# Optimization experiments

Hardware: AMD Instinct MI355X
Metric: run time of the kernel (lower is better)

## Reference

```python
import jax, jax.numpy as jnp
import numpy as np

RATIO = 4
NUM_UPSAMPLES = 2  # log2(RATIO)
PADDING = 11       # (23 - 1) // 2


def _make_kernel():
    cdf23 = 2.0 * np.array([0.5, 0.305334091185, 0.0, -0.072698593239, 0.0,
                            0.021809577942, 0.0, -0.005192756653, 0.0,
                            0.000807762146, 0.0, -6.0081482e-05])
    d = cdf23[::-1]
    base = np.insert(cdf23, 0, d[:-1])  # length 23, symmetric
    return jnp.asarray(base, dtype=jnp.float32)


def setup_inputs() -> dict:
    key = jax.random.key(0)
    x = jax.random.normal(key, (4, 8, 256, 256), dtype=jnp.float32)
    return {"x": x, "kernel": _make_kernel()}


def _sep_circ_conv(img, kernel):
    """Depthwise separable 23-tap conv with circular padding.
    img: (bs, c, h, w). Processes all (b,c) slices as one batched conv."""
    bs, c, h, w = img.shape
    flat = img.reshape(bs * c, 1, h, w)
    # horizontal pass
    ph = jnp.pad(flat, ((0, 0), (0, 0), (0, 0), (PADDING, PADDING)), mode="wrap")
    kh = kernel.reshape(1, 1, 1, -1)
    fh = jax.lax.conv_general_dilated(ph, kh, (1, 1), "VALID",
                                      dimension_numbers=("NCHW", "OIHW", "NCHW"))
    # vertical pass
    pv = jnp.pad(fh, ((0, 0), (0, 0), (PADDING, PADDING), (0, 0)), mode="wrap")
    kv = kernel.reshape(1, 1, -1, 1)
    fv = jax.lax.conv_general_dilated(pv, kv, (1, 1), "VALID",
                                      dimension_numbers=("NCHW", "OIHW", "NCHW"))
    return fv.reshape(bs, c, h, w)


def reference(x, kernel):
    cur = x
    for k in range(NUM_UPSAMPLES):
        bs, c, h, w = cur.shape
        up = jnp.zeros((bs, c, 2 * h, 2 * w), dtype=cur.dtype)
        off = 1 if k == 0 else 0  # first stage inserts at odd positions
        up = up.at[..., off::2, off::2].set(cur)
        cur = _sep_circ_conv(up, kernel)
    return cur
```

## Files before the change

### kernel.cpp

```cpp
#include <hip/hip_runtime.h>


#define SINS 50
#define SMS 132

__global__ void compute_g(const float* __restrict__ kern, float* __restrict__ gbuf) {
    const int u = threadIdx.x;
    const int s = u - 34;
    int jlo = (s - 11 + 1) >> 1;
    int jhi = (s + 11) >> 1;
    if (jlo < -11) jlo = -11;
    if (jhi > 11) jhi = 11;
    float acc = 0.f;
    for (int j = jlo; j <= jhi; ++j)
        acc += kern[11 + s - 2 * j] * kern[11 + j];
    gbuf[u] = acc;
}

__device__ inline void fma4(float4& a, float t, const float4& r) {
    a.x += t * r.x; a.y += t * r.y; a.z += t * r.z; a.w += t * r.w;
}

__global__ __launch_bounds__(256, 4) void up4_fused(
    const float* __restrict__ in, const float* __restrict__ gbuf,
    float* __restrict__ out) {
    __shared__ float sG[80];
    __shared__ __attribute__((aligned(16))) float sMid[49][SMS];
    __shared__ float sIn[49][SINS];

    const int tid = threadIdx.x;
    const int tX = blockIdx.x, tY = blockIdx.y, ch = blockIdx.z;
    const int W4 = 1024;

    if (tid < 80) sG[tid] = gbuf[tid];

    const float* inC = in + (size_t)ch * 256 * 256;
    const int N0y = 32 * tY - 9, N0x = 32 * tX - 9;
#pragma unroll
    for (int it = 0; it < 9; ++it) {
        const int idx = tid + it * 256;
        const int pi = 1 + idx / 48, pj = 1 + idx % 48;
        const int gi = (N0y + pi + 256) & 255;
        const int gj = (N0x + pj + 256) & 255;
        sIn[pi][pj] = inC[gi * 256 + gj];
    }
    __syncthreads();

    float tapA[17], tC6[6];
#pragma unroll
    for (int k = 0; k < 17; ++k) tapA[k] = sG[1 + 4 * k];
#pragma unroll
    for (int m = 0; m < 6; ++m) tC6[m] = sG[12 + 4 * m];

#pragma unroll
    for (int it = 0; it < 6; ++it) {
        const int idx = tid + it * 256;
        const int c = idx & 31, row = 1 + (idx >> 5);
        float a0 = 0.f, a1 = 0.f, a2 = 0.f, a3 = 0.f;
#pragma unroll
        for (int k = 0; k < 17; ++k) {
            const float w = sIn[row][c + 17 - k];
            a1 += tapA[k] * w;
            a3 += tapA[16 - k] * w;
            if (k >= 3 && k <= 14) {
                const int m = k - 3;
                a0 += tC6[m < 6 ? m : 11 - m] * w;
            }
            if (k == 8) a2 = w;
        }
        float4 v; v.x = a0; v.y = a1; v.z = a2; v.w = a3;
        *(float4*)&sMid[row][4 * c] = v;
    }
    __syncthreads();

    const int c = tid & 31, gp = tid >> 5;
    float4 A[4][4];
#pragma unroll
    for (int i = 0; i < 4; ++i)
#pragma unroll
        for (int p = 0; p < 4; ++p) { A[i][p].x = 0.f; A[i][p].y = 0.f; A[i][p].z = 0.f; A[i][p].w = 0.f; }

#pragma unroll
    for (int d = 1; d <= 20; ++d) {
        const float4 R = *(const float4*)&sMid[4 * gp + d][4 * c];
#pragma unroll
        for (int i = 0; i < 4; ++i) {
            const int k = i + 17 - d;
            if (k < 0 || k > 16) continue;
            fma4(A[i][1], tapA[k], R);
            fma4(A[i][3], tapA[16 - k], R);
            if (k >= 3 && k <= 14) {
                const int m = k - 3;
                fma4(A[i][0], tC6[m < 6 ? m : 11 - m], R);
            }
            if (k == 8) A[i][2] = R;
        }
    }

    float* outC = out + (size_t)ch * 1024 * 1024;
    const int row0 = 128 * tY + 16 * gp, col = 128 * tX + 4 * c;
#pragma unroll
    for (int i = 0; i < 4; ++i)
#pragma unroll
        for (int p = 0; p < 4; ++p)
            *(float4*)&outC[(size_t)(row0 + 4 * i + p) * W4 + col] = A[i][p];
}

extern "C" void kernel_launch(void* const* d_in, const int* in_sizes, int n_in,
                              void* d_out, int out_size, void* d_ws, size_t ws_size,
                              hipStream_t stream) {
    const float* x    = (const float*)d_in[0];
    const float* kern = (const float*)d_in[1];
    float* out  = (float*)d_out;
    float* gbuf = (float*)d_ws;

    compute_g<<<dim3(1), dim3(80), 0, stream>>>(kern, gbuf);
    dim3 grid(8, 8, 32);
    up4_fused<<<grid, dim3(256), 0, stream>>>(x, gbuf, out);
}
```

Before: 146.3 us.

## Fold tap precompute into main kernel, vectorize input tile loads and horizontal pass

Drops the separate compute_g launch and has each block compute the combined 80-tap filter into shared memory. Input tiles are loaded with float4 global reads when the tile does not wrap horizontally, with a scalar fallback for wrapped tiles. The horizontal pass now has each thread load a 20-float register window and produce 4 output columns, which cuts shared-memory reads. The shared arrays lose the unused halo row. The trade-off is that every block redundantly recomputes the taps and the window uses more registers.

Result: slower. 149.3 us (+2.0%).

```diff
diff --git a/kernel.cpp b/kernel.cpp
--- a/kernel.cpp
+++ b/kernel.cpp
@@ -1,48 +1,59 @@
 #include <hip/hip_runtime.h>
 
 
-#define SINS 50
+#define SINS 52
 #define SMS 132
-
-__global__ void compute_g(const float* __restrict__ kern, float* __restrict__ gbuf) {
-    const int u = threadIdx.x;
-    const int s = u - 34;
-    int jlo = (s - 11 + 1) >> 1;
-    int jhi = (s + 11) >> 1;
-    if (jlo < -11) jlo = -11;
-    if (jhi > 11) jhi = 11;
-    float acc = 0.f;
-    for (int j = jlo; j <= jhi; ++j)
-        acc += kern[11 + s - 2 * j] * kern[11 + j];
-    gbuf[u] = acc;
-}
 
 __device__ inline void fma4(float4& a, float t, const float4& r) {
     a.x += t * r.x; a.y += t * r.y; a.z += t * r.z; a.w += t * r.w;
 }
 
 __global__ __launch_bounds__(256, 4) void up4_fused(
-    const float* __restrict__ in, const float* __restrict__ gbuf,
+    const float* __restrict__ in, const float* __restrict__ kern,
     float* __restrict__ out) {
     __shared__ float sG[80];
-    __shared__ __attribute__((aligned(16))) float sMid[49][SMS];
-    __shared__ float sIn[49][SINS];
+    __shared__ __attribute__((aligned(16))) float sMid[48][SMS];
+    __shared__ __attribute__((aligned(16))) float sIn[48][SINS];
 
     const int tid = threadIdx.x;
     const int tX = blockIdx.x, tY = blockIdx.y, ch = blockIdx.z;
     const int W4 = 1024;
 
-    if (tid < 80) sG[tid] = gbuf[tid];
+    if (tid < 80) {
+        const int s = tid - 34;
+        int jlo = (s - 10) >> 1;
+        int jhi = (s + 11) >> 1;
+        if (jlo < -11) jlo = -11;
+        if (jhi > 11) jhi = 11;
+        float acc = 0.f;
+        for (int j = jlo; j <= jhi; ++j)
+            acc += kern[11 + s - 2 * j] * kern[11 + j];
+        sG[tid] = acc;
+    }
 
     const float* inC = in + (size_t)ch * 256 * 256;
     const int N0y = 32 * tY - 9, N0x = 32 * tX - 9;
+    const int gj0 = (N0x + 1) & 255;
+    if (gj0 <= 208) {
 #pragma unroll
-    for (int it = 0; it < 9; ++it) {
-        const int idx = tid + it * 256;
-        const int pi = 1 + idx / 48, pj = 1 + idx % 48;
-        const int gi = (N0y + pi + 256) & 255;
-        const int gj = (N0x + pj + 256) & 255;
-        sIn[pi][pj] = inC[gi * 256 + gj];
+        for (int it = 0; it < 3; ++it) {
+            const int idx = tid + it * 256;
+            if (idx < 576) {
+                const int pi = idx / 12, m = idx % 12;
+                const int gi = (N0y + 1 + pi + 256) & 255;
+                *(float4*)&sIn[pi][4 * m] =
+                    *(const float4*)&inC[gi * 256 + gj0 + 4 * m];
+            }
+        }
+    } else {
+#pragma unroll
+        for (int it = 0; it < 9; ++it) {
+            const int idx = tid + it * 256;
+            const int pi = idx / 48, pj = idx % 48;
+            const int gi = (N0y + 1 + pi + 256) & 255;
+            const int gj = (N0x + 1 + pj + 256) & 255;
+            sIn[pi][pj] = inC[gi * 256 + gj];
+        }
     }
     __syncthreads();
 
@@ -53,23 +64,32 @@
     for (int m = 0; m < 6; ++m) tC6[m] = sG[12 + 4 * m];
 
 #pragma unroll
-    for (int it = 0; it < 6; ++it) {
+    for (int it = 0; it < 2; ++it) {
         const int idx = tid + it * 256;
-        const int c = idx & 31, row = 1 + (idx >> 5);
-        float a0 = 0.f, a1 = 0.f, a2 = 0.f, a3 = 0.f;
+        if (idx < 384) {
+            const int t4 = 4 * (idx & 7), row = idx >> 3;
+            float win[20];
 #pragma unroll
-        for (int k = 0; k < 17; ++k) {
-            const float w = sIn[row][c + 17 - k];
-            a1 += tapA[k] * w;
-            a3 += tapA[16 - k] * w;
-            if (k >= 3 && k <= 14) {
-                const int m = k - 3;
-                a0 += tC6[m < 6 ? m : 11 - m] * w;
+            for (int m = 0; m < 5; ++m)
+                *(float4*)&win[4 * m] = *(const float4*)&sIn[row][t4 + 4 * m];
+#pragma unroll
+            for (int q = 0; q < 4; ++q) {
+                float a0 = 0.f, a1 = 0.f, a2 = 0.f, a3 = 0.f;
+#pragma unroll
+                for (int k = 0; k < 17; ++k) {
+                    const float w = win[q + 16 - k];
+                    a1 += tapA[k] * w;
+                    a3 += tapA[16 - k] * w;
+                    if (k >= 3 && k <= 14) {
+                        const int m2 = k - 3;
+                        a0 += tC6[m2 < 6 ? m2 : 11 - m2] * w;
+                    }
+                    if (k == 8) a2 = w;
+                }
+                float4 v; v.x = a0; v.y = a1; v.z = a2; v.w = a3;
+                *(float4*)&sMid[row][4 * (t4 + q)] = v;
             }
-            if (k == 8) a2 = w;
         }
-        float4 v; v.x = a0; v.y = a1; v.z = a2; v.w = a3;
-        *(float4*)&sMid[row][4 * c] = v;
     }
     __syncthreads();
 
@@ -82,7 +102,7 @@
 
 #pragma unroll
     for (int d = 1; d <= 20; ++d) {
-        const float4 R = *(const float4*)&sMid[4 * gp + d][4 * c];
+        const float4 R = *(const float4*)&sMid[4 * gp + d - 1][4 * c];
 #pragma unroll
         for (int i = 0; i < 4; ++i) {
             const int k = i + 17 - d;
@@ -112,9 +132,7 @@
     const float* x    = (const float*)d_in[0];
     const float* kern = (const float*)d_in[1];
     float* out  = (float*)d_out;
-    float* gbuf = (float*)d_ws;
 
-    compute_g<<<dim3(1), dim3(80), 0, stream>>>(kern, gbuf);
     dim3 grid(8, 8, 32);
-    up4_fused<<<grid, dim3(256), 0, stream>>>(x, gbuf, out);
+    up4_fused<<<grid, dim3(256), 0, stream>>>(x, kern, out);
 }
```
